# Kernel optimization log

Measured on AMD Instinct MI355X. Metric: run time of the kernel, lower is better.

The kernel has to match this reference:

```python
import jax, jax.numpy as jnp
import numpy as np

NEG_SLOPE = 0.2  # PyG GATConv default negative_slope


def _gat_layer(x, src, dst, W, a_s, a_d, b, heads, ch):
    N = x.shape[0]
    h = (x @ W).reshape(N, heads, ch)                      # [N,H,C]
    al_s = jnp.sum(h * a_s[None], axis=-1)                 # [N,H]
    al_d = jnp.sum(h * a_d[None], axis=-1)                 # [N,H]
    e = jax.nn.leaky_relu(al_s[src] + al_d[dst], NEG_SLOPE)  # [E,H]
    m = jax.ops.segment_max(e, dst, num_segments=N)        # segment-softmax (stable)
    ex = jnp.exp(e - jax.lax.stop_gradient(m)[dst])
    denom = jax.ops.segment_sum(ex, dst, num_segments=N)
    alpha = ex / (denom[dst] + 1e-16)                      # [E,H]
    msg = h[src] * alpha[..., None]                        # [E,H,C]
    out = jax.ops.segment_sum(msg, dst, num_segments=N)    # [N,H,C]
    return out.reshape(N, heads * ch) + b


def _add_self_loops(edge_index, N):
    loop = jnp.arange(N, dtype=edge_index.dtype)
    src = jnp.concatenate([edge_index[0], loop])
    dst = jnp.concatenate([edge_index[1], loop])
    return src, dst


def gat_forward(x, edge_index, batch, W1, a_src1, a_dst1, b1, W2, a_src2, a_dst2, b2, W3, a_src3, a_dst3, b3, num_graphs=512):
    N = x.shape[0]
    src, dst = _add_self_loops(edge_index, N)
    x = jax.nn.relu(_gat_layer(x, src, dst, W1, a_src1, a_dst1, b1, 4, 64))
    x = jax.nn.relu(_gat_layer(x, src, dst, W2, a_src2, a_dst2, b2, 4, 64))
    x = _gat_layer(x, src, dst, W3, a_src3, a_dst3, b3, 1, 32)
    # global_mean_pool
    sums = jax.ops.segment_sum(x, batch, num_segments=num_graphs)
    cnt = jax.ops.segment_sum(jnp.ones((N,), x.dtype), batch, num_segments=num_graphs)
    return sums / jnp.maximum(cnt, 1.0)[:, None]


def setup_inputs() -> dict:
    key = jax.random.key(0)
    ks = jax.random.split(key, 16)
    N, E, G = 50000, 800000, 512
    IN, HID, H, OUT = 775, 64, 4, 32
    s = 0.05
    return {
        "x": jax.random.normal(ks[0], (N, IN), jnp.float32),
        "edge_index": jax.random.randint(ks[1], (2, E), 0, N, jnp.int32),
        "batch": jnp.sort(jax.random.randint(ks[2], (N,), 0, G, jnp.int32)),
        "W1": jax.random.normal(ks[3], (IN, H * HID), jnp.float32) * s,
        "a_src1": jax.random.normal(ks[4], (H, HID), jnp.float32) * s,
        "a_dst1": jax.random.normal(ks[5], (H, HID), jnp.float32) * s,
        "b1": jnp.zeros((H * HID,), jnp.float32),
        "W2": jax.random.normal(ks[6], (H * HID, H * HID), jnp.float32) * s,
        "a_src2": jax.random.normal(ks[7], (H, HID), jnp.float32) * s,
        "a_dst2": jax.random.normal(ks[8], (H, HID), jnp.float32) * s,
        "b2": jnp.zeros((H * HID,), jnp.float32),
        "W3": jax.random.normal(ks[9], (H * HID, OUT), jnp.float32) * s,
        "a_src3": jax.random.normal(ks[10], (1, OUT), jnp.float32) * s,
        "a_dst3": jax.random.normal(ks[11], (1, OUT), jnp.float32) * s,
        "b3": jnp.zeros((OUT,), jnp.float32),
    }


def reference(x, edge_index, batch, W1, a_src1, a_dst1, b1, W2, a_src2, a_dst2, b2, W3, a_src3, a_dst3, b3):
    return gat_forward(x, edge_index, batch, W1, a_src1, a_dst1, b1, W2, a_src2, a_dst2, b2, W3, a_src3, a_dst3, b3)
```

## Files before the change

kernel.cpp:

```cpp
#include <hip/hip_runtime.h>
#include <hip/hip_bf16.h>

typedef unsigned short u16;
typedef __attribute__((ext_vector_type(4))) unsigned short u16x4;
typedef __attribute__((ext_vector_type(8))) unsigned short u16x8;
typedef __attribute__((ext_vector_type(8))) short bf16x8;
typedef __attribute__((ext_vector_type(4))) float f32x4;

__device__ __forceinline__ u16 f2bs(float f) {
    union { float f; unsigned int u; } x; x.f = f;
    unsigned int r = x.u + 0x7FFFu + ((x.u >> 16) & 1u);
    return (u16)(r >> 16);
}
__device__ __forceinline__ float bs2f(u16 u) {
    union { unsigned int u; float f; } x; x.u = ((unsigned int)u) << 16; return x.f;
}
__device__ __forceinline__ float lrelu(float e) { return e >= 0.f ? e : 0.2f * e; }

__global__ void deg_kernel(const int* __restrict__ dst, int* __restrict__ deg, int E) {
    int i = blockIdx.x * 256 + threadIdx.x;
    if (i < E) atomicAdd(&deg[dst[i]], 1);
}

__global__ __launch_bounds__(1024) void scan_local(const int* __restrict__ deg,
        int* __restrict__ ptr, int* __restrict__ bsum, int N) {
    __shared__ int wsum[16];
    const int t = threadIdx.x, i = blockIdx.x * 1024 + t;
    const int lane = t & 63, w = t >> 6;
    int v = (i < N) ? deg[i] : 0;
    int x = v;
    #pragma unroll
    for (int off = 1; off < 64; off <<= 1) { int y = __shfl_up(x, off); if (lane >= off) x += y; }
    if (lane == 63) wsum[w] = x;
    __syncthreads();
    if (w == 0) {
        int s = (lane < 16) ? wsum[lane] : 0;
        #pragma unroll
        for (int off = 1; off < 16; off <<= 1) { int y = __shfl_up(s, off); if (lane >= off) s += y; }
        if (lane < 16) wsum[lane] = s;
    }
    __syncthreads();
    int incl = x + (w > 0 ? wsum[w - 1] : 0);
    if (i < N) ptr[i + 1] = incl;
    if (t == 0) bsum[blockIdx.x] = wsum[15];
}

__global__ __launch_bounds__(64) void scan_carry(int* __restrict__ bsum, int nb) {
    int t = threadIdx.x;
    int v = (t < nb) ? bsum[t] : 0;
    int x = v;
    #pragma unroll
    for (int off = 1; off < 64; off <<= 1) { int y = __shfl_up(x, off); if (t >= off) x += y; }
    if (t < nb) bsum[t] = x - v;
}

__global__ __launch_bounds__(1024) void scan_final(const int* __restrict__ deg,
        int* __restrict__ ptr, int* __restrict__ cur, const int* __restrict__ bsum, int N) {
    int i = blockIdx.x * 1024 + threadIdx.x;
    if (i == 0) ptr[0] = 0;
    if (i < N) {
        int p = ptr[i + 1] + bsum[blockIdx.x];
        ptr[i + 1] = p;
        cur[i] = p - deg[i];
    }
}

__global__ void fill_kernel(const int* __restrict__ src, const int* __restrict__ dst,
        int* __restrict__ cur, int* __restrict__ csr, int E) {
    int i = blockIdx.x * 256 + threadIdx.x;
    if (i < E) { int p = atomicAdd(&cur[dst[i]], 1); csr[p] = src[i]; }
}

__global__ void bounds_kernel(const int* __restrict__ batch, int* __restrict__ gstart,
        int N, int G) {
    int i = blockIdx.x * 256 + threadIdx.x;
    if (i > N) return;
    if (i == 0) {
        int b0 = batch[0];
        for (int g = 0; g <= b0; g++) gstart[g] = 0;
    } else if (i == N) {
        int bl = batch[N - 1];
        for (int g = bl + 1; g <= G; g++) gstart[g] = N;
    } else {
        int b = batch[i], bp = batch[i - 1];
        for (int g = bp + 1; g <= b; g++) gstart[g] = i;
    }
}

__global__ void transpose_w(const float* __restrict__ W, u16* __restrict__ Wt,
        int K, int Nn, int KT) {
    int idx = blockIdx.x * 256 + threadIdx.x;
    if (idx >= Nn * KT) return;
    int n = idx / KT, k = idx - n * KT;
    Wt[(size_t)n * KT + k] = (k < K) ? f2bs(W[(size_t)k * Nn + n]) : (u16)0;
}

__global__ __launch_bounds__(256) void conv_x(const float* __restrict__ x, u16* __restrict__ xbf) {
    int r = blockIdx.x, t = threadIdx.x;
    const float* row = x + (size_t)r * 775;
    u16* orow = xbf + (size_t)r * 800;
    for (int k = t; k < 800; k += 256)
        orow[k] = (k < 775) ? f2bs(row[k]) : (u16)0;
}

template<bool AFP32>
__global__ __launch_bounds__(256) void gemm128(
        const void* __restrict__ Av, int lda, int M, int K,
        const u16* __restrict__ B, int ldb,
        u16* __restrict__ C, int ldc) {
    const float* Af = (const float*)Av;
    const u16*   Au = (const u16*)Av;
    __shared__ u16 Alds[128][40];
    __shared__ u16 Blds[128][40];
    const int t = threadIdx.x;
    const int row0 = blockIdx.x * 128, col0 = blockIdx.y * 128;
    const int wid = t >> 6, lane = t & 63;
    const int wm = wid >> 1, wn = wid & 1;
    const int quad = lane >> 4, l16 = lane & 15;

    f32x4 acc[4][4];
    f32x4 z = {0.f, 0.f, 0.f, 0.f};
    #pragma unroll
    for (int i = 0; i < 4; i++)
        #pragma unroll
        for (int j = 0; j < 4; j++) acc[i][j] = z;

    const int kTiles = (K + 31) >> 5;
    for (int kt = 0; kt < kTiles; ++kt) {
        const int k0 = kt << 5;
        #pragma unroll
        for (int c = 0; c < 2; c++) {
            int ch = t + c * 256;
            int r = ch >> 2, cp = (ch & 3) * 8;
            int gr = row0 + r;
            u16x8 v = {0,0,0,0,0,0,0,0};
            if (AFP32) {
                #pragma unroll
                for (int u = 0; u < 8; u++) {
                    int k = k0 + cp + u;
                    v[u] = (gr < M && k < K) ? f2bs(Af[(size_t)gr * lda + k]) : (u16)0;
                }
            } else {
                if (gr < M) v = *(const u16x8*)(Au + (size_t)gr * lda + k0 + cp);
            }
            *(u16x8*)&Alds[r][cp] = v;
        }
        #pragma unroll
        for (int c = 0; c < 2; c++) {
            int ch = t + c * 256;
            int r = ch >> 2, cp = (ch & 3) * 8;
            *(u16x8*)&Blds[r][cp] = *(const u16x8*)(B + (size_t)(col0 + r) * ldb + k0 + cp);
        }
        __syncthreads();
        bf16x8 af[4], bfr[4];
        #pragma unroll
        for (int it = 0; it < 4; it++) af[it] = *(const bf16x8*)&Alds[wm * 64 + it * 16 + l16][quad * 8];
        #pragma unroll
        for (int jt = 0; jt < 4; jt++) bfr[jt] = *(const bf16x8*)&Blds[wn * 64 + jt * 16 + l16][quad * 8];
        #pragma unroll
        for (int it = 0; it < 4; it++)
            #pragma unroll
            for (int jt = 0; jt < 4; jt++)
                acc[it][jt] = __builtin_amdgcn_mfma_f32_16x16x32_bf16(af[it], bfr[jt], acc[it][jt], 0, 0, 0);
        __syncthreads();
    }
    #pragma unroll
    for (int it = 0; it < 4; it++) {
        int gr0 = row0 + wm * 64 + it * 16 + quad * 4;
        #pragma unroll
        for (int jt = 0; jt < 4; jt++) {
            int gc = col0 + wn * 64 + jt * 16 + l16;
            #pragma unroll
            for (int r = 0; r < 4; r++) {
                int gr = gr0 + r;
                if (gr < M) C[(size_t)gr * ldc + gc] = f2bs(acc[it][jt][r]);
            }
        }
    }
}

__global__ __launch_bounds__(256) void gemm32(
        const u16* __restrict__ A, int lda, int M, int K,
        const u16* __restrict__ B, int ldb, float* __restrict__ C) {
    __shared__ u16 Alds[128][40];
    __shared__ u16 Blds[32][40];
    const int t = threadIdx.x;
    const int row0 = blockIdx.x * 128;
    const int wid = t >> 6, lane = t & 63;
    const int quad = lane >> 4, l16 = lane & 15;
    f32x4 acc[2][2];
    f32x4 z = {0.f, 0.f, 0.f, 0.f};
    acc[0][0] = z; acc[0][1] = z; acc[1][0] = z; acc[1][1] = z;
    const int kTiles = K >> 5;
    for (int kt = 0; kt < kTiles; ++kt) {
        const int k0 = kt << 5;
        #pragma unroll
        for (int c = 0; c < 2; c++) {
            int ch = t + c * 256;
            int r = ch >> 2, cp = (ch & 3) * 8;
            int gr = row0 + r;
            u16x8 v = {0,0,0,0,0,0,0,0};
            if (gr < M) v = *(const u16x8*)(A + (size_t)gr * lda + k0 + cp);
            *(u16x8*)&Alds[r][cp] = v;
        }
        if (t < 128) {
            int r = t >> 2, cp = (t & 3) * 8;
            *(u16x8*)&Blds[r][cp] = *(const u16x8*)(B + (size_t)r * ldb + k0 + cp);
        }
        __syncthreads();
        bf16x8 af[2], bfr[2];
        #pragma unroll
        for (int it = 0; it < 2; it++) af[it] = *(const bf16x8*)&Alds[wid * 32 + it * 16 + l16][quad * 8];
        #pragma unroll
        for (int jt = 0; jt < 2; jt++) bfr[jt] = *(const bf16x8*)&Blds[jt * 16 + l16][quad * 8];
        #pragma unroll
        for (int it = 0; it < 2; it++)
            #pragma unroll
            for (int jt = 0; jt < 2; jt++)
                acc[it][jt] = __builtin_amdgcn_mfma_f32_16x16x32_bf16(af[it], bfr[jt], acc[it][jt], 0, 0, 0);
        __syncthreads();
    }
    #pragma unroll
    for (int it = 0; it < 2; it++) {
        int gr0 = row0 + wid * 32 + it * 16 + quad * 4;
        #pragma unroll
        for (int jt = 0; jt < 2; jt++) {
            int gc = jt * 16 + l16;
            #pragma unroll
            for (int r = 0; r < 4; r++) {
                int gr = gr0 + r;
                if (gr < M) C[(size_t)gr * 32 + gc] = acc[it][jt][r];
            }
        }
    }
}

__global__ __launch_bounds__(256) void al_kernel(const u16* __restrict__ h,
        const float* __restrict__ a_s, const float* __restrict__ a_d,
        float* __restrict__ als, float* __restrict__ ald, int N) {
    int t = threadIdx.x;
    float as = a_s[t], ad = a_d[t];
    int base = blockIdx.x * 8;
    for (int u = 0; u < 8; u++) {
        int n = base + u;
        if (n >= N) return;
        float hv = bs2f(h[(size_t)n * 256 + t]);
        float ps = hv * as, pd = hv * ad;
        for (int off = 32; off >= 1; off >>= 1) { ps += __shfl_down(ps, off); pd += __shfl_down(pd, off); }
        if ((t & 63) == 0) { int w = t >> 6; als[n * 4 + w] = ps; ald[n * 4 + w] = pd; }
    }
}

__global__ __launch_bounds__(256) void al3_kernel(const float* __restrict__ h3,
        const float* __restrict__ a_s, const float* __restrict__ a_d,
        float* __restrict__ als, float* __restrict__ ald, int N) {
    int t = threadIdx.x, wid = t >> 6, lane = t & 63;
    int c = lane & 31, half = lane >> 5;
    float as = a_s[c], ad = a_d[c];
    int n = blockIdx.x * 8 + wid * 2 + half;
    if (n >= N) return;
    float hv = h3[(size_t)n * 32 + c];
    float ps = hv * as, pd = hv * ad;
    for (int off = 16; off >= 1; off >>= 1) { ps += __shfl_down(ps, off, 32); pd += __shfl_down(pd, off, 32); }
    if (c == 0) { als[n] = ps; ald[n] = pd; }
}

__global__ __launch_bounds__(256) void agg_kernel(const u16* __restrict__ hbuf,
        const float* __restrict__ als, const float* __restrict__ ald,
        const int* __restrict__ ptr, const int* __restrict__ csr,
        const float* __restrict__ bias, u16* __restrict__ act, int N) {
    __shared__ float al_lds[4][64][4];
    __shared__ int   s_lds[4][64];
    const int t = threadIdx.x, wid = t >> 6, lane = t & 63;
    const int i = blockIdx.x * 4 + wid;
    if (i >= N) return;
    const int start = ptr[i], end = ptr[i + 1];
    const int deg = end - start;
    const int head = lane >> 4;

    const f32x4 aldv = *(const f32x4*)&ald[(size_t)i * 4];
    const f32x4 alsv = *(const f32x4*)&als[(size_t)i * 4];
    f32x4 eself;
    #pragma unroll
    for (int hh = 0; hh < 4; hh++) eself[hh] = lrelu(alsv[hh] + aldv[hh]);

    const f32x4 bv = *(const f32x4*)&bias[lane * 4];
    const u16x4 hrs = *(const u16x4*)&hbuf[(size_t)i * 256 + lane * 4];
    f32x4 acc;

    if (deg <= 64) {
        int sreg = 0;
        f32x4 ev;
        #pragma unroll
        for (int hh = 0; hh < 4; hh++) ev[hh] = -1e30f;
        if (lane < deg) {
            sreg = csr[start + lane];
            const f32x4 a = *(const f32x4*)&als[(size_t)sreg * 4];
            #pragma unroll
            for (int hh = 0; hh < 4; hh++) ev[hh] = lrelu(a[hh] + aldv[hh]);
        }
        f32x4 mx;
        #pragma unroll
        for (int hh = 0; hh < 4; hh++) mx[hh] = fmaxf(eself[hh], ev[hh]);
        #pragma unroll
        for (int off = 32; off >= 1; off >>= 1) {
            #pragma unroll
            for (int hh = 0; hh < 4; hh++) mx[hh] = fmaxf(mx[hh], __shfl_xor(mx[hh], off));
        }
        f32x4 sm, av;
        #pragma unroll
        for (int hh = 0; hh < 4; hh++) {
            av[hh] = (lane < deg) ? expf(ev[hh] - mx[hh]) : 0.f;
            sm[hh] = av[hh] + ((lane == 0) ? expf(eself[hh] - mx[hh]) : 0.f);
        }
        #pragma unroll
        for (int off = 32; off >= 1; off >>= 1) {
            #pragma unroll
            for (int hh = 0; hh < 4; hh++) sm[hh] += __shfl_xor(sm[hh], off);
        }
        f32x4 inv;
        #pragma unroll
        for (int hh = 0; hh < 4; hh++) inv[hh] = 1.f / (sm[hh] + 1e-16f);
        #pragma unroll
        for (int hh = 0; hh < 4; hh++) av[hh] *= inv[hh];
        *(f32x4*)&al_lds[wid][lane][0] = av;
        s_lds[wid][lane] = sreg;

        const float aself = expf(eself[head] - mx[head]) * inv[head];
        #pragma unroll
        for (int c2 = 0; c2 < 4; c2++) acc[c2] = aself * bs2f(hrs[c2]);

        int k = 0;
        for (; k + 3 < deg; k += 4) {
            const int s0 = s_lds[wid][k],     s1 = s_lds[wid][k + 1];
            const int s2 = s_lds[wid][k + 2], s3 = s_lds[wid][k + 3];
            const float a0 = al_lds[wid][k][head],     a1 = al_lds[wid][k + 1][head];
            const float a2 = al_lds[wid][k + 2][head], a3 = al_lds[wid][k + 3][head];
            const u16x4 h0 = *(const u16x4*)&hbuf[(size_t)s0 * 256 + lane * 4];
            const u16x4 h1 = *(const u16x4*)&hbuf[(size_t)s1 * 256 + lane * 4];
            const u16x4 h2 = *(const u16x4*)&hbuf[(size_t)s2 * 256 + lane * 4];
            const u16x4 h3v = *(const u16x4*)&hbuf[(size_t)s3 * 256 + lane * 4];
            #pragma unroll
            for (int c2 = 0; c2 < 4; c2++) {
                acc[c2] = fmaf(a0, bs2f(h0[c2]), acc[c2]);
                acc[c2] = fmaf(a1, bs2f(h1[c2]), acc[c2]);
                acc[c2] = fmaf(a2, bs2f(h2[c2]), acc[c2]);
                acc[c2] = fmaf(a3, bs2f(h3v[c2]), acc[c2]);
            }
        }
        for (; k < deg; ++k) {
            const int s = s_lds[wid][k];
            const float a = al_lds[wid][k][head];
            const u16x4 hr = *(const u16x4*)&hbuf[(size_t)s * 256 + lane * 4];
            #pragma unroll
            for (int c2 = 0; c2 < 4; c2++) acc[c2] = fmaf(a, bs2f(hr[c2]), acc[c2]);
        }
    } else {
        f32x4 mx = eself;
        for (int j = start + lane; j < end; j += 64) {
            int s = csr[j];
            const f32x4 a = *(const f32x4*)&als[(size_t)s * 4];
            #pragma unroll
            for (int hh = 0; hh < 4; hh++) mx[hh] = fmaxf(mx[hh], lrelu(a[hh] + aldv[hh]));
        }
        #pragma unroll
        for (int off = 32; off >= 1; off >>= 1) {
            #pragma unroll
            for (int hh = 0; hh < 4; hh++) mx[hh] = fmaxf(mx[hh], __shfl_xor(mx[hh], off));
        }
        f32x4 sm;
        #pragma unroll
        for (int hh = 0; hh < 4; hh++) sm[hh] = (lane == 0) ? expf(eself[hh] - mx[hh]) : 0.f;
        for (int j = start + lane; j < end; j += 64) {
            int s = csr[j];
            const f32x4 a = *(const f32x4*)&als[(size_t)s * 4];
            #pragma unroll
            for (int hh = 0; hh < 4; hh++) sm[hh] += expf(lrelu(a[hh] + aldv[hh]) - mx[hh]);
        }
        #pragma unroll
        for (int off = 32; off >= 1; off >>= 1) {
            #pragma unroll
            for (int hh = 0; hh < 4; hh++) sm[hh] += __shfl_xor(sm[hh], off);
        }
        f32x4 inv;
        #pragma unroll
        for (int hh = 0; hh < 4; hh++) inv[hh] = 1.f / (sm[hh] + 1e-16f);

        const float aself = expf(eself[head] - mx[head]) * inv[head];
        #pragma unroll
        for (int c2 = 0; c2 < 4; c2++) acc[c2] = aself * bs2f(hrs[c2]);

        for (int base = start; base < end; base += 64) {
            const int n64 = min(64, end - base);
            const int j = base + lane;
            int sreg = 0;
            if (j < end) {
                sreg = csr[j];
                const f32x4 a = *(const f32x4*)&als[(size_t)sreg * 4];
                f32x4 alpha;
                #pragma unroll
                for (int hh = 0; hh < 4; hh++)
                    alpha[hh] = expf(lrelu(a[hh] + aldv[hh]) - mx[hh]) * inv[hh];
                *(f32x4*)&al_lds[wid][lane][0] = alpha;
            }
            s_lds[wid][lane] = sreg;
            for (int k = 0; k < n64; ++k) {
                const int s = s_lds[wid][k];
                const float a = al_lds[wid][k][head];
                const u16x4 hr = *(const u16x4*)&hbuf[(size_t)s * 256 + lane * 4];
                #pragma unroll
                for (int c2 = 0; c2 < 4; c2++) acc[c2] = fmaf(a, bs2f(hr[c2]), acc[c2]);
            }
        }
    }

    u16x4 o;
    #pragma unroll
    for (int c2 = 0; c2 < 4; c2++) o[c2] = f2bs(fmaxf(acc[c2] + bv[c2], 0.f));
    *(u16x4*)&act[(size_t)i * 256 + lane * 4] = o;
}

__global__ __launch_bounds__(256) void agg3_kernel(const float* __restrict__ h3,
        const float* __restrict__ als, const float* __restrict__ ald,
        const int* __restrict__ ptr, const int* __restrict__ csr,
        const float* __restrict__ bias, float* __restrict__ out_n, int N) {
    __shared__ float a_lds[4][64];
    __shared__ int   s_lds3[4][64];
    const int t = threadIdx.x, wid = t >> 6, lane = t & 63;
    const int col = lane & 31, half = lane >> 5;
    const int i = blockIdx.x * 4 + wid;
    if (i >= N) return;
    const int start = ptr[i], end = ptr[i + 1];
    const int deg = end - start;
    const float aldv = ald[i];
    const float e0 = lrelu(als[i] + aldv);
    float acc = 0.f;

    if (deg <= 64) {
        int sreg = 0; float ev = -1e30f;
        if (lane < deg) { sreg = csr[start + lane]; ev = lrelu(als[sreg] + aldv); }
        float mx = fmaxf(e0, ev);
        #pragma unroll
        for (int off = 32; off >= 1; off >>= 1) mx = fmaxf(mx, __shfl_xor(mx, off));
        float ex = (lane < deg) ? expf(ev - mx) : 0.f;
        float sm = ex + ((lane == 0) ? expf(e0 - mx) : 0.f);
        #pragma unroll
        for (int off = 32; off >= 1; off >>= 1) sm += __shfl_xor(sm, off);
        const float inv = 1.f / (sm + 1e-16f);
        a_lds[wid][lane] = ex * inv;
        s_lds3[wid][lane] = sreg;
        if (half == 0) acc = expf(e0 - mx) * inv * h3[(size_t)i * 32 + col];

        int k = half;
        for (; k + 6 < deg; k += 8) {
            const int s0 = s_lds3[wid][k],     s1 = s_lds3[wid][k + 2];
            const int s2 = s_lds3[wid][k + 4], s3 = s_lds3[wid][k + 6];
            const float a0 = a_lds[wid][k],     a1 = a_lds[wid][k + 2];
            const float a2 = a_lds[wid][k + 4], a3 = a_lds[wid][k + 6];
            const float v0 = h3[(size_t)s0 * 32 + col];
            const float v1 = h3[(size_t)s1 * 32 + col];
            const float v2 = h3[(size_t)s2 * 32 + col];
            const float v3 = h3[(size_t)s3 * 32 + col];
            acc = fmaf(a0, v0, acc); acc = fmaf(a1, v1, acc);
            acc = fmaf(a2, v2, acc); acc = fmaf(a3, v3, acc);
        }
        for (; k < deg; k += 2)
            acc = fmaf(a_lds[wid][k], h3[(size_t)s_lds3[wid][k] * 32 + col], acc);
    } else {
        float mx = e0;
        for (int j = start + lane; j < end; j += 64)
            mx = fmaxf(mx, lrelu(als[csr[j]] + aldv));
        #pragma unroll
        for (int off = 32; off >= 1; off >>= 1) mx = fmaxf(mx, __shfl_xor(mx, off));
        float sm = (lane == 0) ? expf(e0 - mx) : 0.f;
        for (int j = start + lane; j < end; j += 64)
            sm += expf(lrelu(als[csr[j]] + aldv) - mx);
        #pragma unroll
        for (int off = 32; off >= 1; off >>= 1) sm += __shfl_xor(sm, off);
        const float inv = 1.f / (sm + 1e-16f);
        if (half == 0) acc = expf(e0 - mx) * inv * h3[(size_t)i * 32 + col];
        for (int base = start; base < end; base += 64) {
            const int n64 = min(64, end - base);
            const int j = base + lane;
            int sreg = 0; float av = 0.f;
            if (j < end) {
                sreg = csr[j];
                av = expf(lrelu(als[sreg] + aldv) - mx) * inv;
            }
            a_lds[wid][lane] = av;
            s_lds3[wid][lane] = sreg;
            for (int k = half; k < n64; k += 2)
                acc = fmaf(a_lds[wid][k], h3[(size_t)s_lds3[wid][k] * 32 + col], acc);
        }
    }

    acc += __shfl_down(acc, 32);
    if (half == 0)
        out_n[(size_t)i * 32 + col] = acc + bias[col];
}

__global__ __launch_bounds__(256) void pool_kernel(const float* __restrict__ out_n,
        const int* __restrict__ gstart, float* __restrict__ out, int G) {
    const int t = threadIdx.x, wid = t >> 6, lane = t & 63;
    const int col = lane & 31, half = lane >> 5;
    const int g = blockIdx.x * 4 + wid;
    if (g >= G) return;
    const int s = gstart[g], e = gstart[g + 1];
    float acc = 0.f;
    int r = s + half;
    for (; r + 6 < e; r += 8) {
        acc += out_n[(size_t)r * 32 + col];
        acc += out_n[(size_t)(r + 2) * 32 + col];
        acc += out_n[(size_t)(r + 4) * 32 + col];
        acc += out_n[(size_t)(r + 6) * 32 + col];
    }
    for (; r < e; r += 2) acc += out_n[(size_t)r * 32 + col];
    acc += __shfl_down(acc, 32);
    if (half == 0)
        out[g * 32 + col] = acc / fmaxf((float)(e - s), 1.f);
}

extern "C" void kernel_launch(void* const* d_in, const int* in_sizes, int n_in,
                              void* d_out, int out_size, void* d_ws, size_t ws_size,
                              hipStream_t stream) {
    const int N = 50000, E = 800000, G = 512;
    const float* x    = (const float*)d_in[0];
    const int*   ei   = (const int*)d_in[1];
    const int*   batch= (const int*)d_in[2];
    const float* W1   = (const float*)d_in[3];
    const float* as1  = (const float*)d_in[4];
    const float* ad1  = (const float*)d_in[5];
    const float* b1   = (const float*)d_in[6];
    const float* W2   = (const float*)d_in[7];
    const float* as2  = (const float*)d_in[8];
    const float* ad2  = (const float*)d_in[9];
    const float* b2   = (const float*)d_in[10];
    const float* W3   = (const float*)d_in[11];
    const float* as3  = (const float*)d_in[12];
    const float* ad3  = (const float*)d_in[13];
    const float* b3   = (const float*)d_in[14];
    const int* esrc = ei;
    const int* edst = ei + E;

    char* base = (char*)d_ws; size_t off = 0;
    auto alloc = [&](size_t bytes) -> void* {
        void* p = base + off; off = (off + bytes + 255) & ~(size_t)255; return p;
    };
    u16*   hbuf = (u16*)  alloc((size_t)N * 256 * 2);
    u16*   act  = (u16*)  alloc((size_t)N * 256 * 2);
    float* h3   = (float*)alloc((size_t)N * 32 * 4);
    float* als  = (float*)alloc((size_t)N * 4 * 4);
    float* ald  = (float*)alloc((size_t)N * 4 * 4);
    int*   deg  = (int*)  alloc((size_t)N * 4);
    int*   ptr  = (int*)  alloc((size_t)(N + 1) * 4);
    int*   cur  = (int*)  alloc((size_t)N * 4);
    int*   csr  = (int*)  alloc((size_t)E * 4);
    u16*   Wt   = (u16*)  alloc((size_t)256 * 800 * 2);
    int*   bsum = (int*)  alloc((size_t)64 * 4);
    float* out_n= (float*)alloc((size_t)N * 32 * 4);
    int*   gstart=(int*)  alloc((size_t)(G + 1) * 4);
    u16*   xbf  = (u16*)  alloc((size_t)N * 800 * 2);
    const bool use_xbf = (off <= ws_size);

    hipMemsetAsync(deg, 0, (size_t)N * 4, stream);

    const int nb = (N + 1023) / 1024;
    deg_kernel<<<(E + 255) / 256, 256, 0, stream>>>(edst, deg, E);
    scan_local<<<nb, 1024, 0, stream>>>(deg, ptr, bsum, N);
    scan_carry<<<1, 64, 0, stream>>>(bsum, nb);
    scan_final<<<nb, 1024, 0, stream>>>(deg, ptr, cur, bsum, N);
    fill_kernel<<<(E + 255) / 256, 256, 0, stream>>>(esrc, edst, cur, csr, E);
    bounds_kernel<<<(N + 256) / 256, 256, 0, stream>>>(batch, gstart, N, G);

    dim3 g128((N + 127) / 128, 2);
    const int aggGrid = (N + 3) / 4;
    transpose_w<<<(256 * 800 + 255) / 256, 256, 0, stream>>>(W1, Wt, 775, 256, 800);
    if (use_xbf) {
        conv_x<<<N, 256, 0, stream>>>(x, xbf);
        gemm128<false><<<g128, 256, 0, stream>>>(xbf, 800, N, 775, Wt, 800, hbuf, 256);
    } else {
        gemm128<true><<<g128, 256, 0, stream>>>(x, 775, N, 775, Wt, 800, hbuf, 256);
    }
    al_kernel<<<(N + 7) / 8, 256, 0, stream>>>(hbuf, as1, ad1, als, ald, N);
    agg_kernel<<<aggGrid, 256, 0, stream>>>(hbuf, als, ald, ptr, csr, b1, act, N);
    transpose_w<<<(256 * 256 + 255) / 256, 256, 0, stream>>>(W2, Wt, 256, 256, 256);
    gemm128<false><<<g128, 256, 0, stream>>>(act, 256, N, 256, Wt, 256, hbuf, 256);
    al_kernel<<<(N + 7) / 8, 256, 0, stream>>>(hbuf, as2, ad2, als, ald, N);
    agg_kernel<<<aggGrid, 256, 0, stream>>>(hbuf, als, ald, ptr, csr, b2, act, N);
    transpose_w<<<(32 * 256 + 255) / 256, 256, 0, stream>>>(W3, Wt, 256, 32, 256);
    gemm32<<<(N + 127) / 128, 256, 0, stream>>>(act, 256, N, 256, Wt, 256, h3);
    al3_kernel<<<(N + 7) / 8, 256, 0, stream>>>(h3, as3, ad3, als, ald, N);
    agg3_kernel<<<aggGrid, 256, 0, stream>>>(h3, als, ald, ptr, csr, b3, out_n, N);
    pool_kernel<<<(G + 3) / 4, 256, 0, stream>>>(out_n, gstart, (float*)d_out, G);
}
```

Measured before the change: 705.5 us.

## Widen gathers in GAT aggregation and vectorize conversion and attention-logit kernels

The aggregation kernel now splits each wave into two halves. Each half handles alternate neighbours with 16-byte bf16x8 row loads across 32 lanes, and the partial sums are combined with a cross-half shuffle at the end. The x conversion kernel is flattened so each thread writes four bf16 values at once, and the logit kernel handles two nodes per wave with vector loads and 16-lane reductions. The goal is fewer, wider memory transactions and less reduction overhead. In exchange it adds more registers per lane and a final shuffle, and half the lanes sit idle during the output write.

```diff
diff --git a/kernel.cpp b/kernel.cpp
--- a/kernel.cpp
+++ b/kernel.cpp
@@ -95,12 +95,20 @@
     Wt[(size_t)n * KT + k] = (k < K) ? f2bs(W[(size_t)k * Nn + n]) : (u16)0;
 }
 
-__global__ __launch_bounds__(256) void conv_x(const float* __restrict__ x, u16* __restrict__ xbf) {
-    int r = blockIdx.x, t = threadIdx.x;
+__global__ __launch_bounds__(256) void conv_x(const float* __restrict__ x,
+        u16* __restrict__ xbf, int N) {
+    const int idx = blockIdx.x * 256 + threadIdx.x;
+    if (idx >= N * 200) return;
+    const int r = idx / 200;
+    const int k4 = (idx - r * 200) * 4;
     const float* row = x + (size_t)r * 775;
-    u16* orow = xbf + (size_t)r * 800;
-    for (int k = t; k < 800; k += 256)
-        orow[k] = (k < 775) ? f2bs(row[k]) : (u16)0;
+    u16x4 o;
+    #pragma unroll
+    for (int u = 0; u < 4; u++) {
+        const int k = k4 + u;
+        o[u] = (k < 775) ? f2bs(row[k]) : (u16)0;
+    }
+    *(u16x4*)&xbf[(size_t)r * 800 + k4] = o;
 }
 
 template<bool AFP32>
@@ -238,16 +246,30 @@
 __global__ __launch_bounds__(256) void al_kernel(const u16* __restrict__ h,
         const float* __restrict__ a_s, const float* __restrict__ a_d,
         float* __restrict__ als, float* __restrict__ ald, int N) {
-    int t = threadIdx.x;
-    float as = a_s[t], ad = a_d[t];
-    int base = blockIdx.x * 8;
-    for (int u = 0; u < 8; u++) {
-        int n = base + u;
+    const int t = threadIdx.x, wid = t >> 6, lane = t & 63;
+    const f32x4 as4 = *(const f32x4*)&a_s[lane * 4];
+    const f32x4 ad4 = *(const f32x4*)&a_d[lane * 4];
+    #pragma unroll
+    for (int u = 0; u < 2; u++) {
+        const int n = blockIdx.x * 8 + wid * 2 + u;
         if (n >= N) return;
-        float hv = bs2f(h[(size_t)n * 256 + t]);
-        float ps = hv * as, pd = hv * ad;
-        for (int off = 32; off >= 1; off >>= 1) { ps += __shfl_down(ps, off); pd += __shfl_down(pd, off); }
-        if ((t & 63) == 0) { int w = t >> 6; als[n * 4 + w] = ps; ald[n * 4 + w] = pd; }
+        const u16x4 hv = *(const u16x4*)&h[(size_t)n * 256 + lane * 4];
+        float ps = 0.f, pd = 0.f;
+        #pragma unroll
+        for (int c = 0; c < 4; c++) {
+            const float f = bs2f(hv[c]);
+            ps = fmaf(f, as4[c], ps);
+            pd = fmaf(f, ad4[c], pd);
+        }
+        #pragma unroll
+        for (int off = 8; off >= 1; off >>= 1) {
+            ps += __shfl_xor(ps, off, 16);
+            pd += __shfl_xor(pd, off, 16);
+        }
+        if ((lane & 15) == 0) {
+            als[n * 4 + (lane >> 4)] = ps;
+            ald[n * 4 + (lane >> 4)] = pd;
+        }
     }
 }
 
@@ -276,7 +298,9 @@
     if (i >= N) return;
     const int start = ptr[i], end = ptr[i + 1];
     const int deg = end - start;
-    const int head = lane >> 4;
+    const int col8 = lane & 31;
+    const int half = lane >> 5;
+    const int head8 = col8 >> 3;
 
     const f32x4 aldv = *(const f32x4*)&ald[(size_t)i * 4];
     const f32x4 alsv = *(const f32x4*)&als[(size_t)i * 4];
@@ -284,9 +308,8 @@
     #pragma unroll
     for (int hh = 0; hh < 4; hh++) eself[hh] = lrelu(alsv[hh] + aldv[hh]);
 
-    const f32x4 bv = *(const f32x4*)&bias[lane * 4];
-    const u16x4 hrs = *(const u16x4*)&hbuf[(size_t)i * 256 + lane * 4];
-    f32x4 acc;
+    float acc[8];
+    f32x4 mx, inv;
 
     if (deg <= 64) {
         int sreg = 0;
@@ -299,7 +322,6 @@
             #pragma unroll
             for (int hh = 0; hh < 4; hh++) ev[hh] = lrelu(a[hh] + aldv[hh]);
         }
-        f32x4 mx;
         #pragma unroll
         for (int hh = 0; hh < 4; hh++) mx[hh] = fmaxf(eself[hh], ev[hh]);
         #pragma unroll
@@ -318,7 +340,6 @@
             #pragma unroll
             for (int hh = 0; hh < 4; hh++) sm[hh] += __shfl_xor(sm[hh], off);
         }
-        f32x4 inv;
         #pragma unroll
         for (int hh = 0; hh < 4; hh++) inv[hh] = 1.f / (sm[hh] + 1e-16f);
         #pragma unroll
@@ -326,37 +347,38 @@
         *(f32x4*)&al_lds[wid][lane][0] = av;
         s_lds[wid][lane] = sreg;
 
-        const float aself = expf(eself[head] - mx[head]) * inv[head];
-        #pragma unroll
-        for (int c2 = 0; c2 < 4; c2++) acc[c2] = aself * bs2f(hrs[c2]);
-
-        int k = 0;
-        for (; k + 3 < deg; k += 4) {
-            const int s0 = s_lds[wid][k],     s1 = s_lds[wid][k + 1];
-            const int s2 = s_lds[wid][k + 2], s3 = s_lds[wid][k + 3];
-            const float a0 = al_lds[wid][k][head],     a1 = al_lds[wid][k + 1][head];
-            const float a2 = al_lds[wid][k + 2][head], a3 = al_lds[wid][k + 3][head];
-            const u16x4 h0 = *(const u16x4*)&hbuf[(size_t)s0 * 256 + lane * 4];
-            const u16x4 h1 = *(const u16x4*)&hbuf[(size_t)s1 * 256 + lane * 4];
-            const u16x4 h2 = *(const u16x4*)&hbuf[(size_t)s2 * 256 + lane * 4];
-            const u16x4 h3v = *(const u16x4*)&hbuf[(size_t)s3 * 256 + lane * 4];
-            #pragma unroll
-            for (int c2 = 0; c2 < 4; c2++) {
-                acc[c2] = fmaf(a0, bs2f(h0[c2]), acc[c2]);
-                acc[c2] = fmaf(a1, bs2f(h1[c2]), acc[c2]);
-                acc[c2] = fmaf(a2, bs2f(h2[c2]), acc[c2]);
-                acc[c2] = fmaf(a3, bs2f(h3v[c2]), acc[c2]);
+        const u16x8 hrs = *(const u16x8*)&hbuf[(size_t)i * 256 + col8 * 8];
+        const float aself = expf(eself[head8] - mx[head8]) * inv[head8];
+        #pragma unroll
+        for (int c = 0; c < 8; c++) acc[c] = (half == 0) ? aself * bs2f(hrs[c]) : 0.f;
+
+        int k = half;
+        for (; k + 6 < deg; k += 8) {
+            const int s0 = s_lds[wid][k],     s1 = s_lds[wid][k + 2];
+            const int s2 = s_lds[wid][k + 4], s3 = s_lds[wid][k + 6];
+            const float a0 = al_lds[wid][k][head8],     a1 = al_lds[wid][k + 2][head8];
+            const float a2 = al_lds[wid][k + 4][head8], a3 = al_lds[wid][k + 6][head8];
+            const u16x8 h0 = *(const u16x8*)&hbuf[(size_t)s0 * 256 + col8 * 8];
+            const u16x8 h1 = *(const u16x8*)&hbuf[(size_t)s1 * 256 + col8 * 8];
+            const u16x8 h2 = *(const u16x8*)&hbuf[(size_t)s2 * 256 + col8 * 8];
+            const u16x8 h3v = *(const u16x8*)&hbuf[(size_t)s3 * 256 + col8 * 8];
+            #pragma unroll
+            for (int c = 0; c < 8; c++) {
+                acc[c] = fmaf(a0, bs2f(h0[c]), acc[c]);
+                acc[c] = fmaf(a1, bs2f(h1[c]), acc[c]);
+                acc[c] = fmaf(a2, bs2f(h2[c]), acc[c]);
+                acc[c] = fmaf(a3, bs2f(h3v[c]), acc[c]);
             }
         }
-        for (; k < deg; ++k) {
+        for (; k < deg; k += 2) {
             const int s = s_lds[wid][k];
-            const float a = al_lds[wid][k][head];
-            const u16x4 hr = *(const u16x4*)&hbuf[(size_t)s * 256 + lane * 4];
-            #pragma unroll
-            for (int c2 = 0; c2 < 4; c2++) acc[c2] = fmaf(a, bs2f(hr[c2]), acc[c2]);
+            const float a = al_lds[wid][k][head8];
+            const u16x8 hr = *(const u16x8*)&hbuf[(size_t)s * 256 + col8 * 8];
+            #pragma unroll
+            for (int c = 0; c < 8; c++) acc[c] = fmaf(a, bs2f(hr[c]), acc[c]);
         }
     } else {
-        f32x4 mx = eself;
+        mx = eself;
         for (int j = start + lane; j < end; j += 64) {
             int s = csr[j];
             const f32x4 a = *(const f32x4*)&als[(size_t)s * 4];
@@ -382,13 +404,13 @@
             #pragma unroll
             for (int hh = 0; hh < 4; hh++) sm[hh] += __shfl_xor(sm[hh], off);
         }
-        f32x4 inv;
         #pragma unroll
         for (int hh = 0; hh < 4; hh++) inv[hh] = 1.f / (sm[hh] + 1e-16f);
 
-        const float aself = expf(eself[head] - mx[head]) * inv[head];
-        #pragma unroll
-        for (int c2 = 0; c2 < 4; c2++) acc[c2] = aself * bs2f(hrs[c2]);
+        const u16x8 hrs = *(const u16x8*)&hbuf[(size_t)i * 256 + col8 * 8];
+        const float aself = expf(eself[head8] - mx[head8]) * inv[head8];
+        #pragma unroll
+        for (int c = 0; c < 8; c++) acc[c] = (half == 0) ? aself * bs2f(hrs[c]) : 0.f;
 
         for (int base = start; base < end; base += 64) {
             const int n64 = min(64, end - base);
@@ -404,20 +426,28 @@
                 *(f32x4*)&al_lds[wid][lane][0] = alpha;
             }
             s_lds[wid][lane] = sreg;
-            for (int k = 0; k < n64; ++k) {
+            for (int k = half; k < n64; k += 2) {
                 const int s = s_lds[wid][k];
-                const float a = al_lds[wid][k][head];
-                const u16x4 hr = *(const u16x4*)&hbuf[(size_t)s * 256 + lane * 4];
+                const float a = al_lds[wid][k][head8];
+                const u16x8 hr = *(const u16x8*)&hbuf[(size_t)s * 256 + col8 * 8];
                 #pragma unroll
-                for (int c2 = 0; c2 < 4; c2++) acc[c2] = fmaf(a, bs2f(hr[c2]), acc[c2]);
+                for (int c = 0; c < 8; c++) acc[c] = fmaf(a, bs2f(hr[c]), acc[c]);
             }
         }
     }
 
-    u16x4 o;
-    #pragma unroll
-    for (int c2 = 0; c2 < 4; c2++) o[c2] = f2bs(fmaxf(acc[c2] + bv[c2], 0.f));
-    *(u16x4*)&act[(size_t)i * 256 + lane * 4] = o;
+    #pragma unroll
+    for (int c = 0; c < 8; c++) acc[c] += __shfl_down(acc[c], 32);
+    if (half == 0) {
+        const f32x4 bv0 = *(const f32x4*)&bias[col8 * 8];
+        const f32x4 bv1 = *(const f32x4*)&bias[col8 * 8 + 4];
+        u16x8 o;
+        #pragma unroll
+        for (int c = 0; c < 4; c++) o[c] = f2bs(fmaxf(acc[c] + bv0[c], 0.f));
+        #pragma unroll
+        for (int c = 4; c < 8; c++) o[c] = f2bs(fmaxf(acc[c] + bv1[c - 4], 0.f));
+        *(u16x8*)&act[(size_t)i * 256 + col8 * 8] = o;
+    }
 }
 
 __global__ __launch_bounds__(256) void agg3_kernel(const float* __restrict__ h3,
@@ -576,7 +606,7 @@
     const int aggGrid = (N + 3) / 4;
     transpose_w<<<(256 * 800 + 255) / 256, 256, 0, stream>>>(W1, Wt, 775, 256, 800);
     if (use_xbf) {
-        conv_x<<<N, 256, 0, stream>>>(x, xbf);
+        conv_x<<<(N * 200 + 255) / 256, 256, 0, stream>>>(x, xbf, N);
         gemm128<false><<<g128, 256, 0, stream>>>(xbf, 800, N, 775, Wt, 800, hbuf, 256);
     } else {
         gemm128<true><<<g128, 256, 0, stream>>>(x, 775, N, 775, Wt, 800, hbuf, 256);
```

Result: faster. 639.7 us (-9.3%).
